# Kernel optimization log

Measured on AMD Instinct MI355X. Metric: run time of the kernel, lower is better.

The kernel has to match this reference:

```python
import jax, jax.numpy as jnp
import numpy as np


def setup_inputs() -> dict:
    key = jax.random.key(0)
    k1, k2, kq, kk, kv = jax.random.split(key, 5)
    D = 1024
    N1 = 4096
    N2 = 4096
    s = 1.0 / np.sqrt(D)  # ~ PyTorch Linear init scale
    return {
        "x1": jax.random.normal(k1, (N1, D), dtype=jnp.float32),
        "x2": jax.random.normal(k2, (N2, D), dtype=jnp.float32),
        "Wq": jax.random.uniform(kq, (D, D), dtype=jnp.float32, minval=-s, maxval=s),
        "Wk": jax.random.uniform(kk, (D, D), dtype=jnp.float32, minval=-s, maxval=s),
        "Wv": jax.random.uniform(kv, (D, D), dtype=jnp.float32, minval=-s, maxval=s),
    }


def reference(x1, x2, Wq, Wk, Wv):
    # Linear(input_dim, input_dim, bias=False): y = x @ W^T
    Q = x1 @ Wq.T          # [N1, D]
    K = x2 @ Wk.T          # [N2, D]
    V = x2 @ Wv.T          # [N2, D]
    scores = Q @ K.T       # [N1, N2]  (no 1/sqrt(d) scaling in original)
    weights = jax.nn.softmax(scores, axis=-1)
    return weights @ V     # [N1, D]
```

## Files before the change

kernel.cpp:

```cpp
#include <hip/hip_runtime.h>
#include <cstdint>
#include <cstddef>

typedef _Float16 f16x8 __attribute__((ext_vector_type(8)));
typedef _Float16 f16x4 __attribute__((ext_vector_type(4)));
typedef float f32x4 __attribute__((ext_vector_type(4)));

__device__ __forceinline__ void gload_lds16(const _Float16* g, void* l) {
  __builtin_amdgcn_global_load_lds(
      (const __attribute__((address_space(1))) void*)(g),
      (__attribute__((address_space(3))) void*)(l), 16, 0, 0);
}

struct GDesc {
  const _Float16* A;
  const _Float16* B;
  void* C;
  int lda, ldb, ldc, nbm, nbn;
};

struct SetA { f16x8 b[4]; f16x8 a[4]; };
struct SetB { f16x8 a[4]; };

__device__ __forceinline__ void tile_body(
    int t, int nKT, SetA& cur, SetA& nxt, SetB& sbv, char* smem,
    const _Float16* gA0, const _Float16* gA1,
    const _Float16* gB0, const _Float16* gB1,
    int w, int aBase, int bBase, f32x4 (&acc)[8][4]) {
  asm volatile("s_waitcnt vmcnt(4)" ::: "memory");
  __builtin_amdgcn_s_barrier();
  const int jc = (t + 3 < nKT) ? t + 3 : nKT - 1;
  char* dst = smem + (jc & 3) * 32768;
  gload_lds16(gA0 + jc * 32, dst + (w << 10));
  gload_lds16(gA1 + jc * 32, dst + ((w + 8) << 10));
  gload_lds16(gB0 + jc * 32, dst + 16384 + (w << 10));
  gload_lds16(gB1 + jc * 32, dst + 16384 + ((w + 8) << 10));

  const char* Ab = smem + (t & 3) * 32768;
#pragma unroll
  for (int m = 0; m < 4; ++m)
    sbv.a[m] = *(const f16x8*)(Ab + aBase + ((m + 4) << 10));
  asm volatile("s_waitcnt lgkmcnt(4)" ::: "memory");
  __builtin_amdgcn_sched_barrier(0);

  const char* AbN = smem + ((t + 1) & 3) * 32768;
  const char* BbN = AbN + 16384;
#pragma unroll
  for (int n = 0; n < 4; ++n)
    nxt.b[n] = *(const f16x8*)(BbN + bBase + (n << 10));
#pragma unroll
  for (int m = 0; m < 4; ++m)
    nxt.a[m] = *(const f16x8*)(AbN + aBase + (m << 10));
  __builtin_amdgcn_sched_barrier(0);

  __builtin_amdgcn_s_setprio(1);
#pragma unroll
  for (int m = 0; m < 4; ++m)
#pragma unroll
    for (int n = 0; n < 4; ++n)
      acc[m][n] = __builtin_amdgcn_mfma_f32_16x16x32_f16(cur.a[m], cur.b[n], acc[m][n], 0, 0, 0);
  __builtin_amdgcn_s_setprio(0);
  asm volatile("s_waitcnt lgkmcnt(8)" ::: "memory");
  __builtin_amdgcn_sched_barrier(0);
  __builtin_amdgcn_s_setprio(1);
#pragma unroll
  for (int m = 0; m < 4; ++m)
#pragma unroll
    for (int n = 0; n < 4; ++n)
      acc[m + 4][n] = __builtin_amdgcn_mfma_f32_16x16x32_f16(sbv.a[m], cur.b[n], acc[m + 4][n], 0, 0, 0);
  __builtin_amdgcn_s_setprio(0);
}

template <typename CT, bool MULTI>
__global__ __launch_bounds__(512, 2) void gemmq(
    GDesc d0, GDesc d1, GDesc d2,
    int inner, int nKT, int ksOff, size_t cSplit) {
  __shared__ __align__(16) char smem[131072];

  const int bid = blockIdx.x;
  const int gi  = bid / inner;
  int ib        = bid % inner;

  GDesc d = d0;
  if (MULTI) { if (gi == 1) d = d1; else if (gi == 2) d = d2; }
  const _Float16* A = d.A;
  const _Float16* B = d.B;
  CT* C = (CT*)d.C;
  if (!MULTI) {
    A += (size_t)gi * ksOff;
    B += (size_t)gi * ksOff;
    C += (size_t)gi * cSplit;
  }
  const int lda = d.lda, ldb = d.ldb, ldc = d.ldc, nbn = d.nbn;

  ib = (ib & 7) * (inner >> 3) + (ib >> 3);
  const int brow = (ib / nbn) << 8;
  const int bcol = (ib % nbn) << 8;

  const int tid = threadIdx.x;
  const int w   = tid >> 6;
  const int l   = tid & 63;
  const int wm  = w >> 2;
  const int wn  = w & 3;

  const int sRow = l >> 2;
  const int sCol = (((l & 3) ^ ((l >> 3) & 3)) << 3);
  const _Float16* gA0 = A + (size_t)(brow + (w << 4) + sRow) * lda + sCol;
  const _Float16* gA1 = A + (size_t)(brow + ((w + 8) << 4) + sRow) * lda + sCol;
  const _Float16* gB0 = B + (size_t)(bcol + (w << 4) + sRow) * ldb + sCol;
  const _Float16* gB1 = B + (size_t)(bcol + ((w + 8) << 4) + sRow) * ldb + sCol;

  const int axr = (l >> 1) & 3;
  const int fq  = ((l >> 4) ^ axr) << 4;
  const int aBase = (wm << 13) + ((l & 15) << 6) + fq;
  const int bBase = (wn << 12) + ((l & 15) << 6) + fq;

  f32x4 acc[8][4] = {};
  SetA s0, s1;
  SetB sbv;

#pragma unroll
  for (int tt = 0; tt < 3; ++tt) {
    char* dst = smem + tt * 32768;
    gload_lds16(gA0 + tt * 32, dst + (w << 10));
    gload_lds16(gA1 + tt * 32, dst + ((w + 8) << 10));
    gload_lds16(gB0 + tt * 32, dst + 16384 + (w << 10));
    gload_lds16(gB1 + tt * 32, dst + 16384 + ((w + 8) << 10));
  }
  asm volatile("s_waitcnt vmcnt(8)" ::: "memory");
  __builtin_amdgcn_s_barrier();
  {
    const char* Ab = smem;
    const char* Bb = smem + 16384;
#pragma unroll
    for (int n = 0; n < 4; ++n) s0.b[n] = *(const f16x8*)(Bb + bBase + (n << 10));
#pragma unroll
    for (int m = 0; m < 4; ++m) s0.a[m] = *(const f16x8*)(Ab + aBase + (m << 10));
  }

  for (int t = 0; t < nKT; t += 2) {
    tile_body(t,     nKT, s0, s1, sbv, smem, gA0, gA1, gB0, gB1, w, aBase, bBase, acc);
    tile_body(t + 1, nKT, s1, s0, sbv, smem, gA0, gA1, gB0, gB1, w, aBase, bBase, acc);
  }
  asm volatile("s_waitcnt vmcnt(0) lgkmcnt(0)" ::: "memory");

  const int crow0 = brow + (wm << 7) + ((l >> 4) << 2);
  const int ccol  = bcol + (wn << 6) + (l & 15);
#pragma unroll
  for (int m = 0; m < 8; ++m)
#pragma unroll
    for (int n = 0; n < 4; ++n)
#pragma unroll
      for (int jj = 0; jj < 4; ++jj)
        C[(size_t)(crow0 + (m << 4) + jj) * ldc + ccol + (n << 4)] = (CT)acc[m][n][jj];
}

__global__ __launch_bounds__(256) void softmax_rows(const float* __restrict__ S,
                                                    _Float16* __restrict__ P,
                                                    int N) {
  __shared__ float buf[4096];
  __shared__ float red[8];
  const int row = blockIdx.x;
  const int tid = threadIdx.x;
  const int n4  = N >> 2;
  const float4* s4 = (const float4*)(S + (size_t)row * N);
  float4* b4 = (float4*)buf;

  float m = -3.4e38f;
  for (int i = tid; i < n4; i += 256) {
    float4 v = s4[i];
    b4[i] = v;
    m = fmaxf(m, fmaxf(fmaxf(v.x, v.y), fmaxf(v.z, v.w)));
  }
  for (int off = 32; off > 0; off >>= 1) m = fmaxf(m, __shfl_xor(m, off));
  if ((tid & 63) == 0) red[tid >> 6] = m;
  __syncthreads();
  m = fmaxf(fmaxf(red[0], red[1]), fmaxf(red[2], red[3]));

  float sum = 0.f;
  for (int i = tid; i < n4; i += 256) {
    float4 v = b4[i];
    v.x = __expf(v.x - m); v.y = __expf(v.y - m);
    v.z = __expf(v.z - m); v.w = __expf(v.w - m);
    b4[i] = v;
    sum += (v.x + v.y) + (v.z + v.w);
  }
  for (int off = 32; off > 0; off >>= 1) sum += __shfl_xor(sum, off);
  if ((tid & 63) == 0) red[4 + (tid >> 6)] = sum;
  __syncthreads();
  sum = (red[4] + red[5]) + (red[6] + red[7]);
  const float inv = 1.f / sum;

  f16x4* p4 = (f16x4*)(P + (size_t)row * N);
  for (int i = tid; i < n4; i += 256) {
    float4 v = b4[i];
    f16x4 h = { (_Float16)(v.x * inv), (_Float16)(v.y * inv),
                (_Float16)(v.z * inv), (_Float16)(v.w * inv) };
    p4[i] = h;
  }
}

__global__ __launch_bounds__(256) void cast_f32_f16(const float* __restrict__ in,
                                                    _Float16* __restrict__ out, int n4) {
  int i = blockIdx.x * 256 + threadIdx.x;
  if (i < n4) {
    float4 v = ((const float4*)in)[i];
    f16x4 h = { (_Float16)v.x, (_Float16)v.y, (_Float16)v.z, (_Float16)v.w };
    ((f16x4*)out)[i] = h;
  }
}

__global__ __launch_bounds__(256) void reduce4(const float* __restrict__ p,
                                               float* __restrict__ out,
                                               int n4, size_t stride4) {
  int i = blockIdx.x * 256 + threadIdx.x;
  if (i >= n4) return;
  const float4* p4 = (const float4*)p;
  float4 a = p4[i];
  float4 b = p4[i + stride4];
  float4 c = p4[i + 2 * stride4];
  float4 d = p4[i + 3 * stride4];
  float4 r = { (a.x + b.x) + (c.x + d.x), (a.y + b.y) + (c.y + d.y),
               (a.z + b.z) + (c.z + d.z), (a.w + b.w) + (c.w + d.w) };
  ((float4*)out)[i] = r;
}

extern "C" void kernel_launch(void* const* d_in, const int* in_sizes, int n_in,
                              void* d_out, int out_size, void* d_ws, size_t ws_size,
                              hipStream_t stream) {
  const int D  = 1024;
  const int N1 = in_sizes[0] / D;
  const int N2 = in_sizes[1] / D;

  const float* x1 = (const float*)d_in[0];
  const float* x2 = (const float*)d_in[1];
  const float* Wq = (const float*)d_in[2];
  const float* Wk = (const float*)d_in[3];
  const float* Wv = (const float*)d_in[4];
  float* out = (float*)d_out;

  _Float16* x1h = (_Float16*)d_ws;
  _Float16* x2h = x1h + (size_t)N1 * D;
  _Float16* Wqh = x2h + (size_t)N2 * D;
  _Float16* Wkh = Wqh + (size_t)D * D;
  _Float16* Wvh = Wkh + (size_t)D * D;
  _Float16* Qh  = Wvh + (size_t)D * D;
  _Float16* Kh  = Qh  + (size_t)N1 * D;
  _Float16* Vt  = Kh  + (size_t)N2 * D;
  _Float16* P   = Vt  + (size_t)D * N2;
  float*    S   = (float*)(P + (size_t)N1 * N2);

  auto cast = [&](const float* src, _Float16* dst, size_t n) {
    int n4 = (int)(n >> 2);
    cast_f32_f16<<<dim3((n4 + 255) / 256), 256, 0, stream>>>(src, dst, n4);
  };
  cast(x1, x1h, (size_t)N1 * D);
  cast(x2, x2h, (size_t)N2 * D);
  cast(Wq, Wqh, (size_t)D * D);
  cast(Wk, Wkh, (size_t)D * D);
  cast(Wv, Wvh, (size_t)D * D);

  {
    GDesc dq = { x1h, Wqh, Qh, D, D, D, N1 / 256, D / 256 };
    GDesc dk = { x2h, Wkh, Kh, D, D, D, N2 / 256, D / 256 };
    GDesc dv = { Wvh, x2h, Vt, D, D, N2, D / 256, N2 / 256 };
    gemmq<_Float16, true><<<dim3(192), 512, 0, stream>>>(dq, dk, dv, 64, D / 32, 0, 0);
  }
  {
    GDesc dsd = { Qh, Kh, S, D, D, N2, N1 / 256, N2 / 256 };
    gemmq<float, false><<<dim3(256), 512, 0, stream>>>(dsd, dsd, dsd, 256, D / 32, 0, 0);
  }
  softmax_rows<<<dim3(N1), 256, 0, stream>>>(S, P, N2);
  {
    GDesc dp = { P, Vt, S, N2, N2, D, N1 / 256, D / 256 };
    gemmq<float, false><<<dim3(256), 512, 0, stream>>>(dp, dp, dp, 64, 1024 / 32, 1024,
                                                       (size_t)N1 * D);
  }
  reduce4<<<dim3((N1 * D / 4 + 255) / 256), 256, 0, stream>>>(
      S, out, N1 * D / 4, (size_t)N1 * D / 4);
}
```

Before: 162.4 us.

## Split GEMM tile body into four MFMA quadrants interleaved with loads and barriers

```diff
diff --git a/kernel.cpp b/kernel.cpp
--- a/kernel.cpp
+++ b/kernel.cpp
@@ -19,55 +19,77 @@
   int lda, ldb, ldc, nbm, nbn;
 };
 
-struct SetA { f16x8 b[4]; f16x8 a[4]; };
-struct SetB { f16x8 a[4]; };
+struct QSet { f16x8 a[4]; f16x8 b[2]; };
+
+#define MFMA16(d, va, vb) \
+  d = __builtin_amdgcn_mfma_f32_16x16x32_f16(va, vb, d, 0, 0, 0)
 
 __device__ __forceinline__ void tile_body(
-    int t, int nKT, SetA& cur, SetA& nxt, SetB& sbv, char* smem,
+    int t, int nKT, QSet& cur, QSet& nxt, char* smem,
     const _Float16* gA0, const _Float16* gA1,
     const _Float16* gB0, const _Float16* gB1,
     int w, int aBase, int bBase, f32x4 (&acc)[8][4]) {
-  asm volatile("s_waitcnt vmcnt(4)" ::: "memory");
-  __builtin_amdgcn_s_barrier();
+  const char* Ab = smem + (t & 3) * 32768;
+  const char* Bb = Ab + 16384;
   const int jc = (t + 3 < nKT) ? t + 3 : nKT - 1;
   char* dst = smem + (jc & 3) * 32768;
+  const char* AbN = smem + ((t + 1) & 3) * 32768;
+  const char* BbN = AbN + 16384;
+
+  f16x8 b23[2], a47[4];
+
+  asm volatile("s_waitcnt vmcnt(8)" ::: "memory");
+  __builtin_amdgcn_s_barrier();
   gload_lds16(gA0 + jc * 32, dst + (w << 10));
+  b23[0] = *(const f16x8*)(Bb + bBase + (2 << 10));
+  b23[1] = *(const f16x8*)(Bb + bBase + (3 << 10));
+  asm volatile("s_waitcnt lgkmcnt(2)" ::: "memory");
+  __builtin_amdgcn_sched_barrier(0);
+  __builtin_amdgcn_s_setprio(1);
+#pragma unroll
+  for (int m = 0; m < 4; ++m)
+#pragma unroll
+    for (int n = 0; n < 2; ++n) MFMA16(acc[m][n], cur.a[m], cur.b[n]);
+  __builtin_amdgcn_s_setprio(0);
+
+  __builtin_amdgcn_s_barrier();
   gload_lds16(gA1 + jc * 32, dst + ((w + 8) << 10));
-  gload_lds16(gB0 + jc * 32, dst + 16384 + (w << 10));
-  gload_lds16(gB1 + jc * 32, dst + 16384 + ((w + 8) << 10));
-
-  const char* Ab = smem + (t & 3) * 32768;
-#pragma unroll
-  for (int m = 0; m < 4; ++m)
-    sbv.a[m] = *(const f16x8*)(Ab + aBase + ((m + 4) << 10));
+#pragma unroll
+  for (int m = 0; m < 4; ++m)
+    a47[m] = *(const f16x8*)(Ab + aBase + ((m + 4) << 10));
   asm volatile("s_waitcnt lgkmcnt(4)" ::: "memory");
   __builtin_amdgcn_sched_barrier(0);
-
-  const char* AbN = smem + ((t + 1) & 3) * 32768;
-  const char* BbN = AbN + 16384;
-#pragma unroll
-  for (int n = 0; n < 4; ++n)
+  __builtin_amdgcn_s_setprio(1);
+#pragma unroll
+  for (int m = 0; m < 4; ++m)
+#pragma unroll
+    for (int n = 0; n < 2; ++n) MFMA16(acc[m][n + 2], cur.a[m], b23[n]);
+  __builtin_amdgcn_s_setprio(0);
+
+  __builtin_amdgcn_s_barrier();
+  gload_lds16(gB0 + jc * 32, dst + 16384 + (w << 10));
+#pragma unroll
+  for (int m = 0; m < 4; ++m)
+    nxt.a[m] = *(const f16x8*)(AbN + aBase + (m << 10));
+#pragma unroll
+  for (int n = 0; n < 2; ++n)
     nxt.b[n] = *(const f16x8*)(BbN + bBase + (n << 10));
-#pragma unroll
-  for (int m = 0; m < 4; ++m)
-    nxt.a[m] = *(const f16x8*)(AbN + aBase + (m << 10));
-  __builtin_amdgcn_sched_barrier(0);
-
-  __builtin_amdgcn_s_setprio(1);
-#pragma unroll
-  for (int m = 0; m < 4; ++m)
-#pragma unroll
-    for (int n = 0; n < 4; ++n)
-      acc[m][n] = __builtin_amdgcn_mfma_f32_16x16x32_f16(cur.a[m], cur.b[n], acc[m][n], 0, 0, 0);
-  __builtin_amdgcn_s_setprio(0);
-  asm volatile("s_waitcnt lgkmcnt(8)" ::: "memory");
+  asm volatile("s_waitcnt lgkmcnt(6)" ::: "memory");
   __builtin_amdgcn_sched_barrier(0);
   __builtin_amdgcn_s_setprio(1);
 #pragma unroll
   for (int m = 0; m < 4; ++m)
 #pragma unroll
-    for (int n = 0; n < 4; ++n)
-      acc[m + 4][n] = __builtin_amdgcn_mfma_f32_16x16x32_f16(sbv.a[m], cur.b[n], acc[m + 4][n], 0, 0, 0);
+    for (int n = 0; n < 2; ++n) MFMA16(acc[m + 4][n], a47[m], cur.b[n]);
+  __builtin_amdgcn_s_setprio(0);
+
+  __builtin_amdgcn_s_barrier();
+  gload_lds16(gB1 + jc * 32, dst + 16384 + ((w + 8) << 10));
+  __builtin_amdgcn_s_setprio(1);
+#pragma unroll
+  for (int m = 0; m < 4; ++m)
+#pragma unroll
+    for (int n = 0; n < 2; ++n) MFMA16(acc[m + 4][n + 2], a47[m], b23[n]);
   __builtin_amdgcn_s_setprio(0);
 }
 
@@ -116,8 +138,7 @@
   const int bBase = (wn << 12) + ((l & 15) << 6) + fq;
 
   f32x4 acc[8][4] = {};
-  SetA s0, s1;
-  SetB sbv;
+  QSet s0, s1;
 
 #pragma unroll
   for (int tt = 0; tt < 3; ++tt) {
@@ -133,14 +154,14 @@
     const char* Ab = smem;
     const char* Bb = smem + 16384;
 #pragma unroll
-    for (int n = 0; n < 4; ++n) s0.b[n] = *(const f16x8*)(Bb + bBase + (n << 10));
-#pragma unroll
     for (int m = 0; m < 4; ++m) s0.a[m] = *(const f16x8*)(Ab + aBase + (m << 10));
+#pragma unroll
+    for (int n = 0; n < 2; ++n) s0.b[n] = *(const f16x8*)(Bb + bBase + (n << 10));
   }
 
   for (int t = 0; t < nKT; t += 2) {
-    tile_body(t,     nKT, s0, s1, sbv, smem, gA0, gA1, gB0, gB1, w, aBase, bBase, acc);
-    tile_body(t + 1, nKT, s1, s0, sbv, smem, gA0, gA1, gB0, gB1, w, aBase, bBase, acc);
+    tile_body(t,     nKT, s0, s1, smem, gA0, gA1, gB0, gB1, w, aBase, bBase, acc);
+    tile_body(t + 1, nKT, s1, s0, smem, gA0, gA1, gB0, gB1, w, aBase, bBase, acc);
   }
   asm volatile("s_waitcnt vmcnt(0) lgkmcnt(0)" ::: "memory");
 
```

New measurement: 160.5 us. About the same (-1.2%).
